# Kernel tuning notes

Hardware: AMD Instinct MI355X
Metric: run time of the kernel (lower is better)

The kernel has to match this reference:

```python
import jax, jax.numpy as jnp
import numpy as np

D_MAX = 0.5      # max_dist init kwarg
EPS_W = 1e-8     # weight for far edges
EPS_L = 1e-5     # diagonal jitter on projected Laplacian


def setup_inputs() -> dict:
    key = jax.random.key(0)
    k1, k2, k3, k4, k5 = jax.random.split(key, 5)
    V, d_feat, E, K = 8192, 128, 262144, 512
    # scale so squared distances straddle D_MAX (both branches taken)
    inputs = jax.random.normal(k1, (V, d_feat), dtype=jnp.float32) * 0.05
    src = jax.random.randint(k2, (E,), 0, V)
    off = jax.random.randint(k3, (E,), 1, V)  # avoid self-loops
    dst = (src + off) % V
    edge_index = jnp.stack([src, dst]).astype(jnp.int32)
    A = jax.random.normal(k4, (K, K), dtype=jnp.float32)
    targets = A @ A.T / K + jnp.eye(K, dtype=jnp.float32)  # SPD covariance
    pmat = jax.random.normal(k5, (K, V), dtype=jnp.float32) / np.float32(np.sqrt(V))
    return {"inputs": inputs, "targets": targets, "edge_index": edge_index, "pmat": pmat}


def reference(inputs, targets, edge_index, pmat):
    V = inputs.shape[0]
    K = pmat.shape[0]
    src, dst = edge_index[0], edge_index[1]
    # vectorized per-edge squared distance + thresholded weight
    d = jnp.sum((inputs[src] - inputs[dst]) ** 2, axis=-1)            # [E]
    w = jnp.where(d <= D_MAX, jnp.exp(-d), jnp.float32(EPS_W))        # [E]
    # W = I on diag, w on (i,j) and (j,i) for edges, 0 elsewhere
    W = jnp.eye(V, dtype=inputs.dtype).at[src, dst].set(w).at[dst, src].set(w)
    deg = W.sum(axis=1)                                               # [V]
    idx = jnp.arange(V)
    L = (-W).at[idx, idx].add(deg)                                    # Laplacian D - W
    L_adj = (pmat @ L) @ pmat.T + EPS_L * jnp.eye(K, dtype=inputs.dtype)
    # log det(inv(L_adj)) = -logdet(L_adj); trace(L_adj @ S0) = sum(L_adj * S0^T)
    logdet_Ladj = jnp.linalg.slogdet(L_adj)[1]
    logdet_S0 = jnp.linalg.slogdet(targets)[1]
    tr = jnp.sum(L_adj * targets.T)
    return -logdet_Ladj - logdet_S0 - jnp.float32(K) + tr
```

## Files before the change

### kernel.cpp

```cpp
#include <hip/hip_runtime.h>
#include <math.h>

#define V_N 8192
#define D_F 128
#define E_N 262144
#define K_N 512
#define DMAXF 0.5f
#define EPSW 1e-8f
#define EPSL 1e-5f
#define MAX_SE 16384
#define NZ_SYRK 24
#define L68 68

#define NB_TR 1024
#define NB_CP 256
#define NB_ED (E_N / 32)

__global__ __launch_bounds__(256) void k_pre(const float* __restrict__ P, float* __restrict__ PT,
                                             const float* __restrict__ X, const int* __restrict__ ei,
                                             int* __restrict__ cnt, int* __restrict__ si,
                                             int* __restrict__ sj, float* __restrict__ sw,
                                             unsigned* __restrict__ htab,
                                             const float* __restrict__ T, float* __restrict__ Lw1) {
  int b = blockIdx.x, tid = threadIdx.x;
  if (b < NB_TR) {
    __shared__ float tl[64][65];
    int v0 = (b & 127) * 64, k0 = (b >> 7) * 64;
    int c4 = tid & 15, rq = tid >> 4;
#pragma unroll
    for (int rr = 0; rr < 4; ++rr) {
      int r = rq + 16 * rr;
      float4 f = *(const float4*)&P[(size_t)(k0 + r) * V_N + v0 + c4 * 4];
      tl[r][c4 * 4 + 0] = f.x; tl[r][c4 * 4 + 1] = f.y;
      tl[r][c4 * 4 + 2] = f.z; tl[r][c4 * 4 + 3] = f.w;
    }
    __syncthreads();
#pragma unroll
    for (int rr = 0; rr < 4; ++rr) {
      int r = rq + 16 * rr;
      float4 f;
      f.x = tl[c4 * 4 + 0][r]; f.y = tl[c4 * 4 + 1][r];
      f.z = tl[c4 * 4 + 2][r]; f.w = tl[c4 * 4 + 3][r];
      *(float4*)&PT[(size_t)(v0 + r) * K_N + k0 + c4 * 4] = f;
    }
  } else if (b < NB_TR + NB_CP) {
    int idx = (b - NB_TR) * 256 + tid;
    ((float4*)Lw1)[idx] = ((const float4*)T)[idx];
  } else {
    int t = (b - NB_TR - NB_CP) * 256 + tid;
    int e = t >> 3, lane = t & 7;
    int i = ei[e], j = ei[E_N + e];
    const float4* xi = (const float4*)(X + (size_t)i * D_F);
    const float4* xj = (const float4*)(X + (size_t)j * D_F);
    float4 A0 = xi[lane * 4 + 0], A1 = xi[lane * 4 + 1], A2 = xi[lane * 4 + 2], A3 = xi[lane * 4 + 3];
    float4 B0 = xj[lane * 4 + 0], B1 = xj[lane * 4 + 1], B2 = xj[lane * 4 + 2], B3 = xj[lane * 4 + 3];
    float d = 0.f, dx;
    dx = A0.x - B0.x; d += dx * dx; dx = A0.y - B0.y; d += dx * dx;
    dx = A0.z - B0.z; d += dx * dx; dx = A0.w - B0.w; d += dx * dx;
    dx = A1.x - B1.x; d += dx * dx; dx = A1.y - B1.y; d += dx * dx;
    dx = A1.z - B1.z; d += dx * dx; dx = A1.w - B1.w; d += dx * dx;
    dx = A2.x - B2.x; d += dx * dx; dx = A2.y - B2.y; d += dx * dx;
    dx = A2.z - B2.z; d += dx * dx; dx = A2.w - B2.w; d += dx * dx;
    dx = A3.x - B3.x; d += dx * dx; dx = A3.y - B3.y; d += dx * dx;
    dx = A3.z - B3.z; d += dx * dx; dx = A3.w - B3.w; d += dx * dx;
    d += __shfl_xor(d, 1);
    d += __shfl_xor(d, 2);
    d += __shfl_xor(d, 4);
    if (lane == 0 && d <= DMAXF) {
      float w = expf(-d);
      unsigned a = (unsigned)min(i, j), bb = (unsigned)max(i, j);
      unsigned key = a * 8192u + bb;
      unsigned h = (key * 2654435761u) >> 16;
      bool isnew = false;
      for (int probe = 0; probe < 65536; ++probe) {
        unsigned slot = (h + (unsigned)probe) & 65535u;
        unsigned prev = atomicCAS(&htab[slot], 0u, key);
        if (prev == 0u) { isnew = true; break; }
        if (prev == key) break;
      }
      if (isnew) {
        int p = atomicAdd(cnt, 1);
        if (p < MAX_SE) { si[p] = i; sj[p] = j; sw[p] = w; }
      }
    }
  }
}

__global__ __launch_bounds__(256) void k_syrk(const int* __restrict__ cnt, const int* __restrict__ si,
                                              const int* __restrict__ sj, const float* __restrict__ sw,
                                              const float* __restrict__ PT, float* __restrict__ La,
                                              const float* __restrict__ T, float* __restrict__ tr) {
  int p = blockIdx.x, bj = 0;
  while (p >= 8 - bj) { p -= 8 - bj; ++bj; }
  int bi = bj + p;
  int r0g = bi * 64, c0g = bj * 64;
  int m = min(*cnt, MAX_SE);
  int chunk = (m + NZ_SYRK - 1) / NZ_SYRK;
  int e0 = blockIdx.y * chunk;
  int e1 = min(m, e0 + chunk);

  __shared__ float As[16][68];
  __shared__ float Bs[16][68];
  int tid = threadIdx.x;
  int le = tid >> 4, f = tid & 15;
  int r0 = (tid >> 4) * 4, c0 = (tid & 15) * 4;
  float acc[4][4];
#pragma unroll
  for (int i = 0; i < 4; ++i)
#pragma unroll
    for (int j = 0; j < 4; ++j) acc[i][j] = 0.f;

  float w_ = 0.f;
  float4 ai = make_float4(0.f, 0.f, 0.f, 0.f), aj = ai, ci = ai, cj = ai;
  {
    int e = e0 + le;
    if (e < e1) {
      int i = si[e], j = sj[e];
      w_ = sw[e];
      const float* pi = &PT[(size_t)i * K_N];
      const float* pj = &PT[(size_t)j * K_N];
      ai = *(const float4*)(pi + r0g + f * 4);
      aj = *(const float4*)(pj + r0g + f * 4);
      if (bi != bj) {
        ci = *(const float4*)(pi + c0g + f * 4);
        cj = *(const float4*)(pj + c0g + f * 4);
      }
    }
  }

  for (int es = e0; es < e1; es += 16) {
    float sq = sqrtf(w_);
    float4 qa, qb;
    qa.x = sq * (ai.x - aj.x); qa.y = sq * (ai.y - aj.y);
    qa.z = sq * (ai.z - aj.z); qa.w = sq * (ai.w - aj.w);
    if (bi != bj) {
      qb.x = sq * (ci.x - cj.x); qb.y = sq * (ci.y - cj.y);
      qb.z = sq * (ci.z - cj.z); qb.w = sq * (ci.w - cj.w);
    } else {
      qb = qa;
    }
    __syncthreads();
    *(float4*)&As[le][f * 4] = qa;
    *(float4*)&Bs[le][f * 4] = qb;
    __syncthreads();

    {
      int e = es + 16 + le;
      w_ = 0.f;
      if (e < e1) {
        int i = si[e], j = sj[e];
        w_ = sw[e];
        const float* pi = &PT[(size_t)i * K_N];
        const float* pj = &PT[(size_t)j * K_N];
        ai = *(const float4*)(pi + r0g + f * 4);
        aj = *(const float4*)(pj + r0g + f * 4);
        if (bi != bj) {
          ci = *(const float4*)(pi + c0g + f * 4);
          cj = *(const float4*)(pj + c0g + f * 4);
        }
      }
    }

#pragma unroll
    for (int k = 0; k < 16; ++k) {
      float4 av = *(const float4*)&As[k][r0];
      float4 bv = *(const float4*)&Bs[k][c0];
      acc[0][0] += av.x * bv.x; acc[0][1] += av.x * bv.y; acc[0][2] += av.x * bv.z; acc[0][3] += av.x * bv.w;
      acc[1][0] += av.y * bv.x; acc[1][1] += av.y * bv.y; acc[1][2] += av.y * bv.z; acc[1][3] += av.y * bv.w;
      acc[2][0] += av.z * bv.x; acc[2][1] += av.z * bv.y; acc[2][2] += av.z * bv.z; acc[2][3] += av.z * bv.w;
      acc[3][0] += av.w * bv.x; acc[3][1] += av.w * bv.y; acc[3][2] += av.w * bv.z; acc[3][3] += av.w * bv.w;
    }
  }

  bool addeps = (blockIdx.y == 0) && (bi == bj);
  float tdot = 0.f;
#pragma unroll
  for (int i = 0; i < 4; ++i)
#pragma unroll
    for (int j = 0; j < 4; ++j) {
      float v = acc[i][j];
      int rg = r0g + r0 + i, cg = c0g + c0 + j;
      if (addeps && rg == cg) v += EPSL;
      atomicAdd(&La[(size_t)rg * K_N + cg], v);
      float sc = (bi != bj) ? 2.f : (rg == cg ? 1.f : (rg > cg ? 2.f : 0.f));
      if (sc != 0.f) tdot += sc * v * T[(size_t)rg * K_N + cg];
    }
  tdot += __shfl_down(tdot, 32); tdot += __shfl_down(tdot, 16); tdot += __shfl_down(tdot, 8);
  tdot += __shfl_down(tdot, 4);  tdot += __shfl_down(tdot, 2);  tdot += __shfl_down(tdot, 1);
  if ((tid & 63) == 0) atomicAdd(tr, tdot);
}

__device__ __forceinline__ void factor64_lds(const float* __restrict__ smF, float* A, int j0,
                                             float* __restrict__ ldout, int lane) {
  float a[64];
#pragma unroll
  for (int qq = 0; qq < 16; ++qq) {
    float4 f = *(const float4*)&smF[lane * L68 + qq * 4];
    a[qq * 4 + 0] = f.x; a[qq * 4 + 1] = f.y; a[qq * 4 + 2] = f.z; a[qq * 4 + 3] = f.w;
  }
  float ls = 0.f;
#pragma unroll
  for (int c = 0; c < 64; ++c) {
    float dc = __shfl(a[c], c);
    ls += logf(dc);
    float rs = rsqrtf(dc);
    a[c] *= rs;
#pragma unroll
    for (int k = c + 1; k < 64; ++k)
      a[k] -= a[c] * __shfl(a[c], k);
  }
#pragma unroll
  for (int qq = 0; qq < 16; ++qq) {
    float4 f;
    f.x = a[qq * 4 + 0]; f.y = a[qq * 4 + 1]; f.z = a[qq * 4 + 2]; f.w = a[qq * 4 + 3];
    *(float4*)&A[(size_t)(j0 + lane) * K_N + j0 + qq * 4] = f;
  }
  if (lane == 0) *ldout = ls;
}

__global__ __launch_bounds__(64) void k_fact0(float* La, float* Lw1, float* __restrict__ ld) {
  int m = blockIdx.x;
  float* A = m ? Lw1 : La;
  int lane = threadIdx.x;
  float a[64];
#pragma unroll
  for (int qq = 0; qq < 16; ++qq) {
    float4 f = *(const float4*)&A[(size_t)lane * K_N + qq * 4];
    a[qq * 4 + 0] = f.x; a[qq * 4 + 1] = f.y; a[qq * 4 + 2] = f.z; a[qq * 4 + 3] = f.w;
  }
  float ls = 0.f;
#pragma unroll
  for (int c = 0; c < 64; ++c) {
    float dc = __shfl(a[c], c);
    ls += logf(dc);
    float rs = rsqrtf(dc);
    a[c] *= rs;
#pragma unroll
    for (int k = c + 1; k < 64; ++k)
      a[k] -= a[c] * __shfl(a[c], k);
  }
#pragma unroll
  for (int qq = 0; qq < 16; ++qq) {
    float4 f;
    f.x = a[qq * 4 + 0]; f.y = a[qq * 4 + 1]; f.z = a[qq * 4 + 2]; f.w = a[qq * 4 + 3];
    *(float4*)&A[(size_t)lane * K_N + qq * 4] = f;
  }
  if (lane == 0) ld[m * 8] = ls;
}

__global__ __launch_bounds__(256, 1) void k_cstep(float* La, float* Lw1, float* __restrict__ ld, int s) {
  int m = blockIdx.y;
  float* A = m ? Lw1 : La;
  int tid = threadIdx.x;
  int nt2 = 7 - s;
  int q = blockIdx.x, lbj = 0;
  while (q >= nt2 - lbj) { q -= nt2 - lbj; ++lbj; }
  int lbi = lbj + q;
  int i = s + 1 + lbi, j = s + 1 + lbj;

  __shared__ float LT[64 * L68];
  __shared__ float PiT[64 * L68];
  __shared__ float PjT[64 * L68];
  __shared__ float rinv[64];

  for (int idx = tid; idx < 1024; idx += 256) {
    int r = idx >> 4, cq = (idx & 15) << 2;
    float4 f = *(const float4*)&A[(size_t)(s * 64 + r) * K_N + s * 64 + cq];
    LT[(cq + 0) * L68 + r] = f.x; LT[(cq + 1) * L68 + r] = f.y;
    LT[(cq + 2) * L68 + r] = f.z; LT[(cq + 3) * L68 + r] = f.w;
  }
  __syncthreads();
  if (tid < 64) rinv[tid] = 1.0f / LT[tid * L68 + tid];
  __syncthreads();

  {
    int w = tid >> 6, r = tid & 63;
    bool act = (w == 0) || (w == 1 && i != j);
    if (act) {
      int rowblk = (w == 0) ? i : j;
      const float* src = &A[(size_t)(rowblk * 64 + r) * K_N + s * 64];
      float x[64];
#pragma unroll
      for (int qq = 0; qq < 16; ++qq) {
        float4 f = *(const float4*)(src + qq * 4);
        x[qq * 4 + 0] = f.x; x[qq * 4 + 1] = f.y; x[qq * 4 + 2] = f.z; x[qq * 4 + 3] = f.w;
      }
#pragma unroll
      for (int c = 0; c < 64; ++c) {
        float xc = x[c] * rinv[c];
        x[c] = xc;
#pragma unroll
        for (int k = c + 1; k < 64; ++k)
          x[k] -= xc * LT[c * L68 + k];
      }
      float* dst = (w == 0) ? PiT : PjT;
#pragma unroll
      for (int k = 0; k < 64; ++k) dst[k * L68 + r] = x[k];
    }
  }
  __syncthreads();

  const float* Bp = (i == j) ? PiT : PjT;
  int r0 = (tid >> 4) * 4, c0 = (tid & 15) * 4;
  float acc[4][4];
#pragma unroll
  for (int ii = 0; ii < 4; ++ii)
#pragma unroll
    for (int jj = 0; jj < 4; ++jj) acc[ii][jj] = 0.f;
#pragma unroll 8
  for (int k = 0; k < 64; ++k) {
    float4 av = *(const float4*)&PiT[k * L68 + r0];
    float4 bv = *(const float4*)&Bp[k * L68 + c0];
    acc[0][0] += av.x * bv.x; acc[0][1] += av.x * bv.y; acc[0][2] += av.x * bv.z; acc[0][3] += av.x * bv.w;
    acc[1][0] += av.y * bv.x; acc[1][1] += av.y * bv.y; acc[1][2] += av.y * bv.z; acc[1][3] += av.y * bv.w;
    acc[2][0] += av.z * bv.x; acc[2][1] += av.z * bv.y; acc[2][2] += av.z * bv.z; acc[2][3] += av.z * bv.w;
    acc[3][0] += av.w * bv.x; acc[3][1] += av.w * bv.y; acc[3][2] += av.w * bv.z; acc[3][3] += av.w * bv.w;
  }

  if (i != j || i > s + 1) {
#pragma unroll
    for (int ii = 0; ii < 4; ++ii) {
      float* cp = &A[(size_t)(i * 64 + r0 + ii) * K_N + j * 64 + c0];
      float4 o = *(const float4*)cp;
      float4 wv;
      wv.x = o.x - acc[ii][0]; wv.y = o.y - acc[ii][1];
      wv.z = o.z - acc[ii][2]; wv.w = o.w - acc[ii][3];
      *(float4*)cp = wv;
    }
  } else {
#pragma unroll
    for (int ii = 0; ii < 4; ++ii) {
      const float* cp = &A[(size_t)(i * 64 + r0 + ii) * K_N + i * 64 + c0];
      float4 o = *(const float4*)cp;
      LT[(r0 + ii) * L68 + c0 + 0] = o.x - acc[ii][0];
      LT[(r0 + ii) * L68 + c0 + 1] = o.y - acc[ii][1];
      LT[(r0 + ii) * L68 + c0 + 2] = o.z - acc[ii][2];
      LT[(r0 + ii) * L68 + c0 + 3] = o.w - acc[ii][3];
    }
    __syncthreads();
    if (tid < 64)
      factor64_lds(LT, A, i * 64, &ld[m * 8 + s + 1], tid);
  }
}

__global__ void k_combine(const float* __restrict__ ld, const float* __restrict__ tr, float* __restrict__ out) {
  float l0 = 0.f, l1 = 0.f;
#pragma unroll
  for (int s = 0; s < 8; ++s) { l0 += ld[s]; l1 += ld[8 + s]; }
  out[0] = -l0 - l1 - (float)K_N + tr[0];
}

extern "C" void kernel_launch(void* const* d_in, const int* in_sizes, int n_in,
                              void* d_out, int out_size, void* d_ws, size_t ws_size,
                              hipStream_t stream) {
  const float* X  = (const float*)d_in[0];
  const float* T  = (const float*)d_in[1];
  const int*   ei = (const int*)d_in[2];
  const float* P  = (const float*)d_in[3];
  float* out = (float*)d_out;
  char* ws = (char*)d_ws;

  int*      cnt    = (int*)(ws + 0);
  float*    tr     = (float*)(ws + 16);
  float*    ld     = (float*)(ws + 32);
  unsigned* htab   = (unsigned*)(ws + 4096);
  float*    La     = (float*)(ws + 266240);
  float*    Lw1    = (float*)(ws + 1314816);
  int*      si     = (int*)(ws + 2363392);
  int*      sj     = (int*)(ws + 2428928);
  float*    sw     = (float*)(ws + 2494464);
  float*    PT     = (float*)(ws + 2560000);

  hipMemsetAsync(ws, 0, 1314816, stream);

  k_pre<<<NB_TR + NB_CP + NB_ED, 256, 0, stream>>>(P, PT, X, ei, cnt, si, sj, sw, htab, T, Lw1);
  k_syrk<<<dim3(36, NZ_SYRK), 256, 0, stream>>>(cnt, si, sj, sw, PT, La, T, tr);

  k_fact0<<<2, 64, 0, stream>>>(La, Lw1, ld);
  for (int s = 0; s < 7; ++s) {
    int nt2 = 7 - s;
    k_cstep<<<dim3(nt2 * (nt2 + 1) / 2, 2), 256, 0, stream>>>(La, Lw1, ld, s);
  }
  k_combine<<<1, 1, 0, stream>>>(ld, tr, out);
}
```

Measured before the change: 549.8 us.

## Template cstep by step, fold combine into last step, vectorize trsm LDS reads

Makes the Cholesky step index a template parameter so loop bounds are compile-time constants. It removes the separate combine launch by having the last block of the final step sum the log-dets and write the output, using an atomic completion counter. It also vectorizes the triangular-solve LDS reads as float4, reuses PjT instead of LT as the diagonal staging buffer, and raises the SYRK z-split from 24 to 64. The wider split spreads SYRK work over more blocks but adds more atomic accumulation into La.

```diff
diff --git a/kernel.cpp b/kernel.cpp
--- a/kernel.cpp
+++ b/kernel.cpp
@@ -9,7 +9,7 @@
 #define EPSW 1e-8f
 #define EPSL 1e-5f
 #define MAX_SE 16384
-#define NZ_SYRK 24
+#define NZ_SYRK 64
 #define L68 68
 
 #define NB_TR 1024
@@ -190,14 +190,7 @@
   if ((tid & 63) == 0) atomicAdd(tr, tdot);
 }
 
-__device__ __forceinline__ void factor64_lds(const float* __restrict__ smF, float* A, int j0,
-                                             float* __restrict__ ldout, int lane) {
-  float a[64];
-#pragma unroll
-  for (int qq = 0; qq < 16; ++qq) {
-    float4 f = *(const float4*)&smF[lane * L68 + qq * 4];
-    a[qq * 4 + 0] = f.x; a[qq * 4 + 1] = f.y; a[qq * 4 + 2] = f.z; a[qq * 4 + 3] = f.w;
-  }
+__device__ __forceinline__ float factor64_shfl(float a[64]) {
   float ls = 0.f;
 #pragma unroll
   for (int c = 0; c < 64; ++c) {
@@ -209,6 +202,18 @@
     for (int k = c + 1; k < 64; ++k)
       a[k] -= a[c] * __shfl(a[c], k);
   }
+  return ls;
+}
+
+__device__ __forceinline__ void factor64_lds(const float* __restrict__ smF, float* A, int j0,
+                                             float* __restrict__ ldout, int lane) {
+  float a[64];
+#pragma unroll
+  for (int qq = 0; qq < 16; ++qq) {
+    float4 f = *(const float4*)&smF[lane * L68 + qq * 4];
+    a[qq * 4 + 0] = f.x; a[qq * 4 + 1] = f.y; a[qq * 4 + 2] = f.z; a[qq * 4 + 3] = f.w;
+  }
+  float ls = factor64_shfl(a);
 #pragma unroll
   for (int qq = 0; qq < 16; ++qq) {
     float4 f;
@@ -228,17 +233,7 @@
     float4 f = *(const float4*)&A[(size_t)lane * K_N + qq * 4];
     a[qq * 4 + 0] = f.x; a[qq * 4 + 1] = f.y; a[qq * 4 + 2] = f.z; a[qq * 4 + 3] = f.w;
   }
-  float ls = 0.f;
-#pragma unroll
-  for (int c = 0; c < 64; ++c) {
-    float dc = __shfl(a[c], c);
-    ls += logf(dc);
-    float rs = rsqrtf(dc);
-    a[c] *= rs;
-#pragma unroll
-    for (int k = c + 1; k < 64; ++k)
-      a[k] -= a[c] * __shfl(a[c], k);
-  }
+  float ls = factor64_shfl(a);
 #pragma unroll
   for (int qq = 0; qq < 16; ++qq) {
     float4 f;
@@ -248,15 +243,18 @@
   if (lane == 0) ld[m * 8] = ls;
 }
 
-__global__ __launch_bounds__(256, 1) void k_cstep(float* La, float* Lw1, float* __restrict__ ld, int s) {
+template <int S>
+__global__ __launch_bounds__(256, 1) void k_cstep(float* La, float* Lw1, float* __restrict__ ld,
+                                                  const float* __restrict__ tr, float* __restrict__ out,
+                                                  unsigned* __restrict__ donec) {
   int m = blockIdx.y;
   float* A = m ? Lw1 : La;
   int tid = threadIdx.x;
-  int nt2 = 7 - s;
+  constexpr int nt2 = 7 - S;
   int q = blockIdx.x, lbj = 0;
   while (q >= nt2 - lbj) { q -= nt2 - lbj; ++lbj; }
   int lbi = lbj + q;
-  int i = s + 1 + lbi, j = s + 1 + lbj;
+  int i = S + 1 + lbi, j = S + 1 + lbj;
 
   __shared__ float LT[64 * L68];
   __shared__ float PiT[64 * L68];
@@ -265,7 +263,7 @@
 
   for (int idx = tid; idx < 1024; idx += 256) {
     int r = idx >> 4, cq = (idx & 15) << 2;
-    float4 f = *(const float4*)&A[(size_t)(s * 64 + r) * K_N + s * 64 + cq];
+    float4 f = *(const float4*)&A[(size_t)(S * 64 + r) * K_N + S * 64 + cq];
     LT[(cq + 0) * L68 + r] = f.x; LT[(cq + 1) * L68 + r] = f.y;
     LT[(cq + 2) * L68 + r] = f.z; LT[(cq + 3) * L68 + r] = f.w;
   }
@@ -278,7 +276,7 @@
     bool act = (w == 0) || (w == 1 && i != j);
     if (act) {
       int rowblk = (w == 0) ? i : j;
-      const float* src = &A[(size_t)(rowblk * 64 + r) * K_N + s * 64];
+      const float* src = &A[(size_t)(rowblk * 64 + r) * K_N + S * 64];
       float x[64];
 #pragma unroll
       for (int qq = 0; qq < 16; ++qq) {
@@ -289,9 +287,15 @@
       for (int c = 0; c < 64; ++c) {
         float xc = x[c] * rinv[c];
         x[c] = xc;
-#pragma unroll
-        for (int k = c + 1; k < 64; ++k)
-          x[k] -= xc * LT[c * L68 + k];
+        int kk = c + 1;
+#pragma unroll
+        for (; kk < 64 && (kk & 3); ++kk) x[kk] -= xc * LT[c * L68 + kk];
+#pragma unroll
+        for (; kk < 64; kk += 4) {
+          float4 f = *(const float4*)&LT[c * L68 + kk];
+          x[kk + 0] -= xc * f.x; x[kk + 1] -= xc * f.y;
+          x[kk + 2] -= xc * f.z; x[kk + 3] -= xc * f.w;
+        }
       }
       float* dst = (w == 0) ? PiT : PjT;
 #pragma unroll
@@ -317,7 +321,7 @@
     acc[3][0] += av.w * bv.x; acc[3][1] += av.w * bv.y; acc[3][2] += av.w * bv.z; acc[3][3] += av.w * bv.w;
   }
 
-  if (i != j || i > s + 1) {
+  if (i != j || i > S + 1) {
 #pragma unroll
     for (int ii = 0; ii < 4; ++ii) {
       float* cp = &A[(size_t)(i * 64 + r0 + ii) * K_N + j * 64 + c0];
@@ -332,22 +336,30 @@
     for (int ii = 0; ii < 4; ++ii) {
       const float* cp = &A[(size_t)(i * 64 + r0 + ii) * K_N + i * 64 + c0];
       float4 o = *(const float4*)cp;
-      LT[(r0 + ii) * L68 + c0 + 0] = o.x - acc[ii][0];
-      LT[(r0 + ii) * L68 + c0 + 1] = o.y - acc[ii][1];
-      LT[(r0 + ii) * L68 + c0 + 2] = o.z - acc[ii][2];
-      LT[(r0 + ii) * L68 + c0 + 3] = o.w - acc[ii][3];
+      PjT[(r0 + ii) * L68 + c0 + 0] = o.x - acc[ii][0];
+      PjT[(r0 + ii) * L68 + c0 + 1] = o.y - acc[ii][1];
+      PjT[(r0 + ii) * L68 + c0 + 2] = o.z - acc[ii][2];
+      PjT[(r0 + ii) * L68 + c0 + 3] = o.w - acc[ii][3];
     }
     __syncthreads();
     if (tid < 64)
-      factor64_lds(LT, A, i * 64, &ld[m * 8 + s + 1], tid);
-  }
-}
-
-__global__ void k_combine(const float* __restrict__ ld, const float* __restrict__ tr, float* __restrict__ out) {
-  float l0 = 0.f, l1 = 0.f;
-#pragma unroll
-  for (int s = 0; s < 8; ++s) { l0 += ld[s]; l1 += ld[8 + s]; }
-  out[0] = -l0 - l1 - (float)K_N + tr[0];
+      factor64_lds(PjT, A, i * 64, &ld[m * 8 + S + 1], tid);
+
+    if constexpr (S == 6) {
+      if (tid == 0) {
+        __threadfence();
+        unsigned old = __hip_atomic_fetch_add(donec, 1u, __ATOMIC_ACQ_REL, __HIP_MEMORY_SCOPE_AGENT);
+        if (old == 1u) {
+          float lsum = 0.f;
+#pragma unroll
+          for (int t = 0; t < 16; ++t)
+            lsum += __hip_atomic_load(&ld[t], __ATOMIC_ACQUIRE, __HIP_MEMORY_SCOPE_AGENT);
+          float trv = __hip_atomic_load(tr, __ATOMIC_ACQUIRE, __HIP_MEMORY_SCOPE_AGENT);
+          out[0] = -lsum - (float)K_N + trv;
+        }
+      }
+    }
+  }
 }
 
 extern "C" void kernel_launch(void* const* d_in, const int* in_sizes, int n_in,
@@ -363,6 +375,7 @@
   int*      cnt    = (int*)(ws + 0);
   float*    tr     = (float*)(ws + 16);
   float*    ld     = (float*)(ws + 32);
+  unsigned* donec  = (unsigned*)(ws + 192);
   unsigned* htab   = (unsigned*)(ws + 4096);
   float*    La     = (float*)(ws + 266240);
   float*    Lw1    = (float*)(ws + 1314816);
@@ -377,9 +390,11 @@
   k_syrk<<<dim3(36, NZ_SYRK), 256, 0, stream>>>(cnt, si, sj, sw, PT, La, T, tr);
 
   k_fact0<<<2, 64, 0, stream>>>(La, Lw1, ld);
-  for (int s = 0; s < 7; ++s) {
-    int nt2 = 7 - s;
-    k_cstep<<<dim3(nt2 * (nt2 + 1) / 2, 2), 256, 0, stream>>>(La, Lw1, ld, s);
-  }
-  k_combine<<<1, 1, 0, stream>>>(ld, tr, out);
-}
+  k_cstep<0><<<dim3(28, 2), 256, 0, stream>>>(La, Lw1, ld, tr, out, donec);
+  k_cstep<1><<<dim3(21, 2), 256, 0, stream>>>(La, Lw1, ld, tr, out, donec);
+  k_cstep<2><<<dim3(15, 2), 256, 0, stream>>>(La, Lw1, ld, tr, out, donec);
+  k_cstep<3><<<dim3(10, 2), 256, 0, stream>>>(La, Lw1, ld, tr, out, donec);
+  k_cstep<4><<<dim3(6, 2), 256, 0, stream>>>(La, Lw1, ld, tr, out, donec);
+  k_cstep<5><<<dim3(3, 2), 256, 0, stream>>>(La, Lw1, ld, tr, out, donec);
+  k_cstep<6><<<dim3(1, 2), 256, 0, stream>>>(La, Lw1, ld, tr, out, donec);
+}
```

After: 911.2 us. 1.66x slower.
